# Performance work log

Hardware: AMD Instinct MI355X
Metric: run time of the kernel (lower is better)

Reference implementation:

```python
import jax, jax.numpy as jnp
import numpy as np

HEADS = 16
DIM_HEAD = 64
RMS_EPS = 1e-12  # torch F.normalize default eps


def setup_inputs() -> dict:
    key = jax.random.key(0)
    k1, k2, k3 = jax.random.split(key, 3)
    b, n, dim = 2, 2048, 1024
    dim_inner = HEADS * DIM_HEAD
    x = jax.random.normal(k1, (b, n, dim), dtype=jnp.float32)
    gamma = jnp.ones((dim,), dtype=jnp.float32)
    w_qkv = jax.random.normal(k2, (dim, 3 * dim_inner), dtype=jnp.float32) * (dim ** -0.5)
    w_out = jax.random.normal(k3, (dim_inner, dim), dtype=jnp.float32) * (dim_inner ** -0.5)
    return {"x": x, "gamma": gamma, "w_qkv": w_qkv, "w_out": w_out}


def reference(x, gamma, w_qkv, w_out):
    b, n, dim = x.shape
    h, d = HEADS, DIM_HEAD
    # RMSNorm: F.normalize(x, dim=-1) * sqrt(dim) * gamma
    l2 = jnp.maximum(jnp.linalg.norm(x, axis=-1, keepdims=True), RMS_EPS)
    normed = x / l2 * (dim ** 0.5) * gamma
    # qkv projection, split order: (qkv h d)
    qkv = (normed @ w_qkv).reshape(b, n, 3, h, d)
    qkv = jnp.transpose(qkv, (2, 0, 3, 1, 4))  # [3, b, h, n, d]
    q, k, v = qkv[0], qkv[1], qkv[2]
    q = q * (d ** -0.5)
    sim = jnp.einsum('bhid,bhjd->bhij', q, k)  # [b,h,n,n]
    mask_value = -jnp.finfo(sim.dtype).max
    causal_mask = jnp.triu(jnp.ones((n, n), dtype=bool), k=1)
    sim = jnp.where(causal_mask, mask_value, sim)
    attn = jax.nn.softmax(sim, axis=-1)
    out = jnp.einsum('bhij,bhjd->bhid', attn, v)  # [b,h,n,d]
    out = jnp.transpose(out, (0, 2, 1, 3)).reshape(b, n, h * d)
    return out @ w_out
```

## Files before the change

### kernel.cpp

```cpp
#include <hip/hip_runtime.h>
#include <hip/hip_bf16.h>

#define BATCH 2
#define SEQ 2048
#define DMODEL 1024
#define NHEAD 16
#define DHEAD 64
#define NQKV 3072
#define DINNER 1024

typedef __attribute__((ext_vector_type(4))) short short4v;
typedef __attribute__((ext_vector_type(8))) short short8v;
typedef __attribute__((ext_vector_type(4))) float f32x4;

__device__ __forceinline__ unsigned short f2bf(float f) {
  union { float f; unsigned int u; } c; c.f = f;
  unsigned int u = c.u;
  u += 0x7fffu + ((u >> 16) & 1u);
  return (unsigned short)(u >> 16);
}

__device__ __forceinline__ short8v load_frag(const unsigned short* p0, const unsigned short* p1) {
  union { short8v v8; short4v v4[2]; } u;
  u.v4[0] = *(const short4v*)p0;
  u.v4[1] = *(const short4v*)p1;
  return u.v8;
}

#define GL16(gp, lp)                                             \
  __builtin_amdgcn_global_load_lds(                              \
      (__attribute__((address_space(1))) void*)(gp),             \
      (__attribute__((address_space(3))) void*)(lp), 16, 0, 0)

__global__ __launch_bounds__(256) void transpose_cast_kernel(const float* __restrict__ in,
                                                             unsigned short* __restrict__ out,
                                                             int K, int N) {
  __shared__ float tile[32][33];
  const int tiles_n = N >> 5;
  const int tn = blockIdx.x % tiles_n;
  const int tk = blockIdx.x / tiles_n;
  const int k0 = tk << 5, n0 = tn << 5;
  const int t = threadIdx.x;
#pragma unroll
  for (int p = 0; p < 4; p++) {
    const int e = p * 256 + t;
    const int r = e >> 5, c = e & 31;
    tile[r][c] = in[(size_t)(k0 + r) * N + n0 + c];
  }
  __syncthreads();
#pragma unroll
  for (int p = 0; p < 4; p++) {
    const int e = p * 256 + t;
    const int r = e >> 5, c = e & 31;
    out[(size_t)(n0 + r) * K + k0 + c] = f2bf(tile[c][r]);
  }
}

__global__ __launch_bounds__(256) void rmsnorm_kernel(const float* __restrict__ x,
                                                      const float* __restrict__ gamma,
                                                      unsigned short* __restrict__ out) {
  const int row = blockIdx.x;
  const int t = threadIdx.x;
  const float* xr = x + (size_t)row * DMODEL;
  float4 v = ((const float4*)xr)[t];
  float ss = v.x * v.x + v.y * v.y + v.z * v.z + v.w * v.w;
#pragma unroll
  for (int off = 1; off < 64; off <<= 1) ss += __shfl_xor(ss, off);
  __shared__ float wss[4];
  if ((t & 63) == 0) wss[t >> 6] = ss;
  __syncthreads();
  const float tot = wss[0] + wss[1] + wss[2] + wss[3];
  float l2 = sqrtf(tot);
  l2 = fmaxf(l2, 1e-12f);
  const float s = 32.0f / l2;
  const float4 gm = ((const float4*)gamma)[t];
  unsigned short o[4];
  o[0] = f2bf(v.x * s * gm.x);
  o[1] = f2bf(v.y * s * gm.y);
  o[2] = f2bf(v.z * s * gm.z);
  o[3] = f2bf(v.w * s * gm.w);
  unsigned short* op = out + (size_t)row * DMODEL + t * 4;
  *(short4v*)op = *(short4v*)o;
}

#define BM 128
#define BN 128
#define BKT 32
#define TILE_E (BM * BKT)

__device__ void gemm_core(const unsigned short* __restrict__ A,
                          const unsigned short* __restrict__ Bt, int K, int rowBase,
                          int colBase, unsigned short* sA, unsigned short* sB,
                          f32x4 acc[4][4]) {
  const int t = threadIdx.x;
  const int lane = t & 63, wave = t >> 6;
  const int l15 = lane & 15, g = lane >> 4;
  const int wr = (wave >> 1) * 64, wc = (wave & 1) * 64;
#pragma unroll
  for (int m = 0; m < 4; m++)
#pragma unroll
    for (int n = 0; n < 4; n++) acc[m][n] = (f32x4){0.f, 0.f, 0.f, 0.f};
  const int r0 = t >> 2, o0 = (t & 3) * 8;
  const unsigned short* Ag0 = A + (size_t)(rowBase + r0) * K + o0;
  const unsigned short* Ag1 = A + (size_t)(rowBase + r0 + 64) * K + o0;
  const unsigned short* Bg0 = Bt + (size_t)(colBase + r0) * K + o0;
  const unsigned short* Bg1 = Bt + (size_t)(colBase + r0 + 64) * K + o0;
  GL16(Ag0, sA + t * 8);
  GL16(Ag1, sA + (t + 256) * 8);
  GL16(Bg0, sB + t * 8);
  GL16(Bg1, sB + (t + 256) * 8);
  __syncthreads();
  int cur = 0;
  for (int k0 = 0; k0 < K; k0 += BKT, cur ^= 1) {
    if (k0 + BKT < K) {
      const int nxto = (cur ^ 1) * TILE_E;
      GL16(Ag0 + k0 + BKT, sA + nxto + t * 8);
      GL16(Ag1 + k0 + BKT, sA + nxto + (t + 256) * 8);
      GL16(Bg0 + k0 + BKT, sB + nxto + t * 8);
      GL16(Bg1 + k0 + BKT, sB + nxto + (t + 256) * 8);
    }
    const unsigned short* sAc = sA + cur * TILE_E;
    const unsigned short* sBc = sB + cur * TILE_E;
    short8v af[4], bf[4];
#pragma unroll
    for (int m = 0; m < 4; m++)
      af[m] = *(const short8v*)(sAc + (wr + m * 16 + l15) * BKT + 8 * g);
#pragma unroll
    for (int n = 0; n < 4; n++)
      bf[n] = *(const short8v*)(sBc + (wc + n * 16 + l15) * BKT + 8 * g);
#pragma unroll
    for (int m = 0; m < 4; m++)
#pragma unroll
      for (int n = 0; n < 4; n++)
        acc[m][n] = __builtin_amdgcn_mfma_f32_16x16x32_bf16(af[m], bf[n], acc[m][n], 0, 0, 0);
    __syncthreads();
  }
}

__global__ __launch_bounds__(256) void qkv_gemm_kernel(const unsigned short* __restrict__ A,
                                                       const unsigned short* __restrict__ Bt,
                                                       unsigned short* __restrict__ qb,
                                                       unsigned short* __restrict__ kb,
                                                       unsigned short* __restrict__ vtb) {
  __shared__ __align__(16) unsigned short sA[2 * TILE_E];
  __shared__ __align__(16) unsigned short sB[2 * TILE_E];
  const int nbn = NQKV / BN;
  const int bm = blockIdx.x / nbn, bn = blockIdx.x % nbn;
  f32x4 acc[4][4];
  gemm_core(A, Bt, DMODEL, bm * BM, bn * BN, sA, sB, acc);
  const int t = threadIdx.x, lane = t & 63, wave = t >> 6;
  const int l15 = lane & 15, g = lane >> 4;
  const int wr = (wave >> 1) * 64, wc = (wave & 1) * 64;
#pragma unroll
  for (int m = 0; m < 4; m++)
#pragma unroll
    for (int n = 0; n < 4; n++) {
      const int col = bn * BN + wc + n * 16 + l15;
      const int part = col >> 10;
      const int h = (col >> 6) & 15;
      const int d = col & 63;
      const int row0 = bm * BM + wr + m * 16 + 4 * g;
      const int bb = row0 >> 11, i0 = row0 & 2047;
      if (part == 2) {
        union { short4v v; unsigned short u[4]; } pk;
#pragma unroll
        for (int r = 0; r < 4; r++) pk.u[r] = f2bf(acc[m][n][r]);
        *(short4v*)(vtb + ((size_t)(bb * NHEAD + h) * DHEAD + d) * SEQ + i0) = pk.v;
      } else {
#pragma unroll
        for (int r = 0; r < 4; r++) {
          const size_t idx = (((size_t)(bb * NHEAD + h)) * SEQ + i0 + r) * DHEAD + d;
          const float v = acc[m][n][r];
          if (part == 0) qb[idx] = f2bf(v * 0.125f);
          else kb[idx] = f2bf(v);
        }
      }
    }
}

__global__ __launch_bounds__(256) void out_gemm_kernel(const unsigned short* __restrict__ A,
                                                       const unsigned short* __restrict__ Bt,
                                                       float* __restrict__ C) {
  __shared__ __align__(16) unsigned short sA[2 * TILE_E];
  __shared__ __align__(16) unsigned short sB[2 * TILE_E];
  const int nbn = DMODEL / BN;
  const int bm = blockIdx.x / nbn, bn = blockIdx.x % nbn;
  f32x4 acc[4][4];
  gemm_core(A, Bt, DINNER, bm * BM, bn * BN, sA, sB, acc);
  const int t = threadIdx.x, lane = t & 63, wave = t >> 6;
  const int l15 = lane & 15, g = lane >> 4;
  const int wr = (wave >> 1) * 64, wc = (wave & 1) * 64;
#pragma unroll
  for (int m = 0; m < 4; m++)
#pragma unroll
    for (int n = 0; n < 4; n++) {
      const int col = bn * BN + wc + n * 16 + l15;
#pragma unroll
      for (int r = 0; r < 4; r++) {
        const int row = bm * BM + wr + m * 16 + 4 * g + r;
        C[(size_t)row * DMODEL + col] = acc[m][n][r];
      }
    }
}

__global__ __launch_bounds__(256, 4) void attn_kernel(const unsigned short* __restrict__ qb,
                                                      const unsigned short* __restrict__ kb,
                                                      const unsigned short* __restrict__ vtb,
                                                      unsigned short* __restrict__ ob) {
  __shared__ __align__(16) unsigned short sK[2][64 * 64];
  __shared__ __align__(16) unsigned short sV[2][64 * 72];
  const int t = threadIdx.x, lane = t & 63, wave = t >> 6;
  const int l15 = lane & 15, g = lane >> 4;
  const int bh = blockIdx.x & 31;
  const int qord = blockIdx.x >> 5;
  const int qblk = (qord < 8) ? 31 - qord
                 : (qord < 16) ? qord - 8
                 : (qord < 24) ? 39 - qord
                 : qord - 16;
  const int qrow = qblk * 64 + wave * 16 + l15;
  const unsigned short* qptr = qb + (size_t)bh * SEQ * DHEAD;
  const unsigned short* kptr = kb + (size_t)bh * SEQ * DHEAD;
  const unsigned short* vtptr = vtb + (size_t)bh * DHEAD * SEQ;

  const int kr0 = t >> 3, kj0 = ((t & 7) ^ (kr0 & 7)) * 8;
  const int kr1 = (t + 256) >> 3, kj1 = ((t & 7) ^ (kr1 & 7)) * 8;
  const int vr0 = t >> 3, vo0 = (t & 7) * 8;
  const int vr1 = (t + 256) >> 3, vo1 = (t & 7) * 8;

  short8v qf[2];
#pragma unroll
  for (int kk = 0; kk < 2; kk++)
    qf[kk] = *(const short8v*)(qptr + (size_t)qrow * DHEAD + kk * 32 + 8 * g);

  float rm = -__builtin_inff();
  float rl = 0.f;
  f32x4 acc_o[4];
#pragma unroll
  for (int df = 0; df < 4; df++) acc_o[df] = (f32x4){0.f, 0.f, 0.f, 0.f};

  const int nsteps = qblk + 1;

  GL16(kptr + (size_t)kr0 * DHEAD + kj0, sK[0] + t * 8);
  GL16(kptr + (size_t)kr1 * DHEAD + kj1, sK[0] + (t + 256) * 8);
  {
    short8v va = *(const short8v*)(vtptr + (size_t)vr0 * SEQ + vo0);
    short8v vb = *(const short8v*)(vtptr + (size_t)vr1 * SEQ + vo1);
    *(short8v*)(sV[0] + vr0 * 72 + vo0) = va;
    *(short8v*)(sV[0] + vr1 * 72 + vo1) = vb;
  }
  __syncthreads();

  int cur = 0;
  for (int s = 0; s < nsteps; ++s, cur ^= 1) {
    const int nxt = cur ^ 1;
    const bool more = (s + 1 < nsteps);
    short8v va, vb;
    if (more) {
      const int k0n = (s + 1) * 64;
      GL16(kptr + (size_t)(k0n + kr0) * DHEAD + kj0, sK[nxt] + t * 8);
      GL16(kptr + (size_t)(k0n + kr1) * DHEAD + kj1, sK[nxt] + (t + 256) * 8);
      va = *(const short8v*)(vtptr + (size_t)vr0 * SEQ + k0n + vo0);
      vb = *(const short8v*)(vtptr + (size_t)vr1 * SEQ + k0n + vo1);
    }
    {
      const int k0 = s * 64;
      const unsigned short* sKc = sK[cur];
      const unsigned short* sVc = sV[cur];
      short8v kf[4][2];
#pragma unroll
      for (int n4 = 0; n4 < 4; n4++) {
        const int row = n4 * 16 + l15;
#pragma unroll
        for (int kk = 0; kk < 2; kk++)
          kf[n4][kk] = *(const short8v*)(sKc + row * 64 + (((kk * 4 + g) ^ (row & 7)) * 8));
      }
      f32x4 s4[4];
#pragma unroll
      for (int n4 = 0; n4 < 4; n4++) s4[n4] = (f32x4){0.f, 0.f, 0.f, 0.f};
#pragma unroll
      for (int n4 = 0; n4 < 4; n4++)
#pragma unroll
        for (int kk = 0; kk < 2; kk++)
          s4[n4] = __builtin_amdgcn_mfma_f32_16x16x32_bf16(kf[n4][kk], qf[kk],
                                                           s4[n4], 0, 0, 0);
      if (s == nsteps - 1) {
#pragma unroll
        for (int n4 = 0; n4 < 4; n4++)
#pragma unroll
          for (int r = 0; r < 4; r++)
            if (k0 + n4 * 16 + 4 * g + r > qrow) s4[n4][r] = -__builtin_inff();
      }
      float mx = s4[0][0];
#pragma unroll
      for (int n4 = 0; n4 < 4; n4++)
#pragma unroll
        for (int r = 0; r < 4; r++)
          if (n4 || r) mx = fmaxf(mx, s4[n4][r]);
      if (!__all(mx <= rm)) {
        mx = fmaxf(mx, __shfl_xor(mx, 16));
        mx = fmaxf(mx, __shfl_xor(mx, 32));
        const float nm = fmaxf(rm, mx);
        const float al = __expf(rm - nm);
        rm = nm;
        rl *= al;
#pragma unroll
        for (int df = 0; df < 4; df++)
#pragma unroll
          for (int r = 0; r < 4; r++) acc_o[df][r] *= al;
      }
#pragma unroll
      for (int n4 = 0; n4 < 4; n4++)
#pragma unroll
        for (int r = 0; r < 4; r++) {
          const float e = __expf(s4[n4][r] - rm);
          s4[n4][r] = e;
          rl += e;
        }
      unsigned int pw[8];
#pragma unroll
      for (int n4 = 0; n4 < 4; n4++) {
        asm("v_cvt_pk_bf16_f32 %0, %1, %2"
            : "=v"(pw[n4 * 2]) : "v"(s4[n4][0]), "v"(s4[n4][1]));
        asm("v_cvt_pk_bf16_f32 %0, %1, %2"
            : "=v"(pw[n4 * 2 + 1]) : "v"(s4[n4][2]), "v"(s4[n4][3]));
      }
      union { short8v v; unsigned int wd[4]; } paA, paB;
      paA.wd[0] = pw[0]; paA.wd[1] = pw[1]; paA.wd[2] = pw[2]; paA.wd[3] = pw[3];
      paB.wd[0] = pw[4]; paB.wd[1] = pw[5]; paB.wd[2] = pw[6]; paB.wd[3] = pw[7];
#pragma unroll
      for (int df = 0; df < 4; df++) {
        const unsigned short* pv0 = sVc + (df * 16 + l15) * 72 + 4 * g;
        const short8v vfa = load_frag(pv0, pv0 + 16);
        acc_o[df] = __builtin_amdgcn_mfma_f32_16x16x32_bf16(vfa, paA.v, acc_o[df], 0, 0, 0);
        const unsigned short* pv1 = pv0 + 32;
        const short8v vfb = load_frag(pv1, pv1 + 16);
        acc_o[df] = __builtin_amdgcn_mfma_f32_16x16x32_bf16(vfb, paB.v, acc_o[df], 0, 0, 0);
      }
    }
    if (more) {
      *(short8v*)(sV[nxt] + vr0 * 72 + vo0) = va;
      *(short8v*)(sV[nxt] + vr1 * 72 + vo1) = vb;
    }
    __syncthreads();
  }

  const int bb = bh >> 4, hh = bh & 15;
  float ps = rl;
  ps += __shfl_xor(ps, 16);
  ps += __shfl_xor(ps, 32);
  const float inv = 1.0f / ps;
#pragma unroll
  for (int df = 0; df < 4; df++) {
    union { short4v v; unsigned short u[4]; } pk4;
#pragma unroll
    for (int r = 0; r < 4; r++) pk4.u[r] = f2bf(acc_o[df][r] * inv);
    *(short4v*)(ob + ((size_t)bb * SEQ + qrow) * DINNER + hh * DHEAD + df * 16 + 4 * g) =
        pk4.v;
  }
}

extern "C" void kernel_launch(void* const* d_in, const int* in_sizes, int n_in,
                              void* d_out, int out_size, void* d_ws, size_t ws_size,
                              hipStream_t stream) {
  (void)in_sizes; (void)n_in; (void)out_size; (void)ws_size;
  const float* x = (const float*)d_in[0];
  const float* gamma = (const float*)d_in[1];
  const float* w_qkv = (const float*)d_in[2];
  const float* w_out = (const float*)d_in[3];
  float* out = (float*)d_out;
  char* ws = (char*)d_ws;
  unsigned short* wqkvT = (unsigned short*)(ws);
  unsigned short* woutT = (unsigned short*)(ws + 6291456);
  unsigned short* normed = (unsigned short*)(ws + 8388608);
  unsigned short* qbuf = (unsigned short*)(ws + 16777216);
  unsigned short* kbuf = (unsigned short*)(ws + 25165824);
  unsigned short* vtbuf = (unsigned short*)(ws + 33554432);
  unsigned short* aout = (unsigned short*)(ws + 41943040);

  hipLaunchKernelGGL(transpose_cast_kernel, dim3((DMODEL / 32) * (NQKV / 32)), dim3(256), 0,
                     stream, w_qkv, wqkvT, DMODEL, NQKV);
  hipLaunchKernelGGL(transpose_cast_kernel, dim3((DINNER / 32) * (DMODEL / 32)), dim3(256), 0,
                     stream, w_out, woutT, DINNER, DMODEL);
  hipLaunchKernelGGL(rmsnorm_kernel, dim3(BATCH * SEQ), dim3(256), 0, stream, x, gamma, normed);
  hipLaunchKernelGGL(qkv_gemm_kernel, dim3((BATCH * SEQ / BM) * (NQKV / BN)), dim3(256), 0,
                     stream, normed, wqkvT, qbuf, kbuf, vtbuf);
  hipLaunchKernelGGL(attn_kernel, dim3(BATCH * NHEAD * 32), dim3(256), 0, stream,
                     qbuf, kbuf, vtbuf, aout);
  hipLaunchKernelGGL(out_gemm_kernel, dim3((BATCH * SEQ / BM) * (DMODEL / BN)), dim3(256), 0,
                     stream, aout, woutT, out);
}
```

Measured before the change: 112.6 us.

## Use 128-row query blocks with 512 threads, exp2 softmax, and MFMA row sums

The attention kernel now processes 128 query rows per block with 8 waves. Each block loads one K/V tile of 64 keys per step and shares it across twice as many queries, which halves the global and LDS traffic per query. The per-wave step limit skips tiles that lie fully above the causal diagonal for the first four waves. Q is pre-scaled by log2(e)/8 so the softmax can use the hardware v_exp_f32 (base-2) instruction directly. The running row sum is accumulated with an MFMA against a ones vector instead of scalar adds and cross-lane shuffles. In exchange, blocks are larger and fewer, which may hurt occupancy or load balance, and the ones-MFMA adds matrix work.

```diff
diff --git a/kernel.cpp b/kernel.cpp
--- a/kernel.cpp
+++ b/kernel.cpp
@@ -18,6 +18,12 @@
   unsigned int u = c.u;
   u += 0x7fffu + ((u >> 16) & 1u);
   return (unsigned short)(u >> 16);
+}
+
+__device__ __forceinline__ float exp2_hw(float x) {
+  float r;
+  asm("v_exp_f32 %0, %1" : "=v"(r) : "v"(x));
+  return r;
 }
 
 __device__ __forceinline__ short8v load_frag(const unsigned short* p0, const unsigned short* p1) {
@@ -171,7 +177,7 @@
         for (int r = 0; r < 4; r++) {
           const size_t idx = (((size_t)(bb * NHEAD + h)) * SEQ + i0 + r) * DHEAD + d;
           const float v = acc[m][n][r];
-          if (part == 0) qb[idx] = f2bf(v * 0.125f);
+          if (part == 0) qb[idx] = f2bf(v * 0.18033688f);
           else kb[idx] = f2bf(v);
         }
       }
@@ -203,7 +209,7 @@
     }
 }
 
-__global__ __launch_bounds__(256, 4) void attn_kernel(const unsigned short* __restrict__ qb,
+__global__ __launch_bounds__(512, 4) void attn_kernel(const unsigned short* __restrict__ qb,
                                                       const unsigned short* __restrict__ kb,
                                                       const unsigned short* __restrict__ vtb,
                                                       unsigned short* __restrict__ ob) {
@@ -213,40 +219,37 @@
   const int l15 = lane & 15, g = lane >> 4;
   const int bh = blockIdx.x & 31;
   const int qord = blockIdx.x >> 5;
-  const int qblk = (qord < 8) ? 31 - qord
-                 : (qord < 16) ? qord - 8
-                 : (qord < 24) ? 39 - qord
-                 : qord - 16;
-  const int qrow = qblk * 64 + wave * 16 + l15;
+  const int qblk = (qord < 8) ? 15 - qord : qord - 8;
+  const int qrow = qblk * 128 + wave * 16 + l15;
   const unsigned short* qptr = qb + (size_t)bh * SEQ * DHEAD;
   const unsigned short* kptr = kb + (size_t)bh * SEQ * DHEAD;
   const unsigned short* vtptr = vtb + (size_t)bh * DHEAD * SEQ;
 
-  const int kr0 = t >> 3, kj0 = ((t & 7) ^ (kr0 & 7)) * 8;
-  const int kr1 = (t + 256) >> 3, kj1 = ((t & 7) ^ (kr1 & 7)) * 8;
-  const int vr0 = t >> 3, vo0 = (t & 7) * 8;
-  const int vr1 = (t + 256) >> 3, vo1 = (t & 7) * 8;
+  const int kr = t >> 3, kj = ((t & 7) ^ (kr & 7)) * 8;
+  const int vr = t >> 3, vo = (t & 7) * 8;
 
   short8v qf[2];
 #pragma unroll
   for (int kk = 0; kk < 2; kk++)
     qf[kk] = *(const short8v*)(qptr + (size_t)qrow * DHEAD + kk * 32 + 8 * g);
 
+  union { short8v v; unsigned short u[8]; } ones;
+#pragma unroll
+  for (int j = 0; j < 8; j++) ones.u[j] = 0x3F80;
+
   float rm = -__builtin_inff();
-  float rl = 0.f;
+  f32x4 acc_l = (f32x4){0.f, 0.f, 0.f, 0.f};
   f32x4 acc_o[4];
 #pragma unroll
   for (int df = 0; df < 4; df++) acc_o[df] = (f32x4){0.f, 0.f, 0.f, 0.f};
 
-  const int nsteps = qblk + 1;
-
-  GL16(kptr + (size_t)kr0 * DHEAD + kj0, sK[0] + t * 8);
-  GL16(kptr + (size_t)kr1 * DHEAD + kj1, sK[0] + (t + 256) * 8);
+  const int nsteps = 2 * qblk + 2;
+  const int smax_w = 2 * qblk + (wave >> 2);
+
+  GL16(kptr + (size_t)kr * DHEAD + kj, sK[0] + t * 8);
   {
-    short8v va = *(const short8v*)(vtptr + (size_t)vr0 * SEQ + vo0);
-    short8v vb = *(const short8v*)(vtptr + (size_t)vr1 * SEQ + vo1);
-    *(short8v*)(sV[0] + vr0 * 72 + vo0) = va;
-    *(short8v*)(sV[0] + vr1 * 72 + vo1) = vb;
+    short8v va = *(const short8v*)(vtptr + (size_t)vr * SEQ + vo);
+    *(short8v*)(sV[0] + vr * 72 + vo) = va;
   }
   __syncthreads();
 
@@ -254,15 +257,13 @@
   for (int s = 0; s < nsteps; ++s, cur ^= 1) {
     const int nxt = cur ^ 1;
     const bool more = (s + 1 < nsteps);
-    short8v va, vb;
+    short8v va;
     if (more) {
       const int k0n = (s + 1) * 64;
-      GL16(kptr + (size_t)(k0n + kr0) * DHEAD + kj0, sK[nxt] + t * 8);
-      GL16(kptr + (size_t)(k0n + kr1) * DHEAD + kj1, sK[nxt] + (t + 256) * 8);
-      va = *(const short8v*)(vtptr + (size_t)vr0 * SEQ + k0n + vo0);
-      vb = *(const short8v*)(vtptr + (size_t)vr1 * SEQ + k0n + vo1);
-    }
-    {
+      GL16(kptr + (size_t)(k0n + kr) * DHEAD + kj, sK[nxt] + t * 8);
+      va = *(const short8v*)(vtptr + (size_t)vr * SEQ + k0n + vo);
+    }
+    if (s <= smax_w) {
       const int k0 = s * 64;
       const unsigned short* sKc = sK[cur];
       const unsigned short* sVc = sV[cur];
@@ -283,7 +284,7 @@
         for (int kk = 0; kk < 2; kk++)
           s4[n4] = __builtin_amdgcn_mfma_f32_16x16x32_bf16(kf[n4][kk], qf[kk],
                                                            s4[n4], 0, 0, 0);
-      if (s == nsteps - 1) {
+      if (s == smax_w) {
 #pragma unroll
         for (int n4 = 0; n4 < 4; n4++)
 #pragma unroll
@@ -300,9 +301,10 @@
         mx = fmaxf(mx, __shfl_xor(mx, 16));
         mx = fmaxf(mx, __shfl_xor(mx, 32));
         const float nm = fmaxf(rm, mx);
-        const float al = __expf(rm - nm);
+        const float al = exp2_hw(rm - nm);
         rm = nm;
-        rl *= al;
+#pragma unroll
+        for (int r = 0; r < 4; r++) acc_l[r] *= al;
 #pragma unroll
         for (int df = 0; df < 4; df++)
 #pragma unroll
@@ -311,11 +313,7 @@
 #pragma unroll
       for (int n4 = 0; n4 < 4; n4++)
 #pragma unroll
-        for (int r = 0; r < 4; r++) {
-          const float e = __expf(s4[n4][r] - rm);
-          s4[n4][r] = e;
-          rl += e;
-        }
+        for (int r = 0; r < 4; r++) s4[n4][r] = exp2_hw(s4[n4][r] - rm);
       unsigned int pw[8];
 #pragma unroll
       for (int n4 = 0; n4 < 4; n4++) {
@@ -327,6 +325,8 @@
       union { short8v v; unsigned int wd[4]; } paA, paB;
       paA.wd[0] = pw[0]; paA.wd[1] = pw[1]; paA.wd[2] = pw[2]; paA.wd[3] = pw[3];
       paB.wd[0] = pw[4]; paB.wd[1] = pw[5]; paB.wd[2] = pw[6]; paB.wd[3] = pw[7];
+      acc_l = __builtin_amdgcn_mfma_f32_16x16x32_bf16(ones.v, paA.v, acc_l, 0, 0, 0);
+      acc_l = __builtin_amdgcn_mfma_f32_16x16x32_bf16(ones.v, paB.v, acc_l, 0, 0, 0);
 #pragma unroll
       for (int df = 0; df < 4; df++) {
         const unsigned short* pv0 = sVc + (df * 16 + l15) * 72 + 4 * g;
@@ -337,18 +337,12 @@
         acc_o[df] = __builtin_amdgcn_mfma_f32_16x16x32_bf16(vfb, paB.v, acc_o[df], 0, 0, 0);
       }
     }
-    if (more) {
-      *(short8v*)(sV[nxt] + vr0 * 72 + vo0) = va;
-      *(short8v*)(sV[nxt] + vr1 * 72 + vo1) = vb;
-    }
+    if (more) *(short8v*)(sV[nxt] + vr * 72 + vo) = va;
     __syncthreads();
   }
 
   const int bb = bh >> 4, hh = bh & 15;
-  float ps = rl;
-  ps += __shfl_xor(ps, 16);
-  ps += __shfl_xor(ps, 32);
-  const float inv = 1.0f / ps;
+  const float inv = 1.0f / acc_l[0];
 #pragma unroll
   for (int df = 0; df < 4; df++) {
     union { short4v v; unsigned short u[4]; } pk4;
@@ -384,7 +378,7 @@
   hipLaunchKernelGGL(rmsnorm_kernel, dim3(BATCH * SEQ), dim3(256), 0, stream, x, gamma, normed);
   hipLaunchKernelGGL(qkv_gemm_kernel, dim3((BATCH * SEQ / BM) * (NQKV / BN)), dim3(256), 0,
                      stream, normed, wqkvT, qbuf, kbuf, vtbuf);
-  hipLaunchKernelGGL(attn_kernel, dim3(BATCH * NHEAD * 32), dim3(256), 0, stream,
+  hipLaunchKernelGGL(attn_kernel, dim3(BATCH * NHEAD * 16), dim3(512), 0, stream,
                      qbuf, kbuf, vtbuf, aout);
   hipLaunchKernelGGL(out_gemm_kernel, dim3((BATCH * SEQ / BM) * (DMODEL / BN)), dim3(256), 0,
                      stream, aout, woutT, out);
```

After: 119.2 us. 5.8% more time.
